# Kernel tuning notes

Hardware: AMD Instinct MI355X
Metric: run time of the kernel (lower is better)

## Reference

```python
import jax, jax.numpy as jnp
import numpy as np

B, S, D = 2, 2048, 1024
H, A = 16, 64  # num_heads, attention_dim


def setup_inputs() -> dict:
    key = jax.random.key(0)
    ks = jax.random.split(key, 9)
    sd = D ** -0.5
    so = (H * A) ** -0.5
    return {
        "x": jax.random.normal(ks[0], (B, S, D), dtype=jnp.float32),
        "Wq": jax.random.normal(ks[1], (D, H * A), dtype=jnp.float32) * sd,
        "bq": jnp.zeros((H * A,), dtype=jnp.float32),
        "Wk": jax.random.normal(ks[2], (D, H * A), dtype=jnp.float32) * sd,
        "bk": jnp.zeros((H * A,), dtype=jnp.float32),
        "Wv": jax.random.normal(ks[3], (D, H * A), dtype=jnp.float32) * sd,
        "bv": jnp.zeros((H * A,), dtype=jnp.float32),
        "Wo": jax.random.normal(ks[4], (H * A, D), dtype=jnp.float32) * so,
        "bo": jnp.zeros((D,), dtype=jnp.float32),
    }


def reference(x, Wq, bq, Wk, bk, Wv, bv, Wo, bo):
    b, s, _ = x.shape
    # project and split heads: [b, s, H, A]
    q = (x @ Wq + bq).reshape(b, s, H, A)
    k = (x @ Wk + bk).reshape(b, s, H, A)
    v = (x @ Wv + bv).reshape(b, s, H, A)
    # scores [b, H, s, s]
    scores = jnp.einsum("bqhd,bkhd->bhqk", q, k) / jnp.sqrt(jnp.float32(A))
    weights = jax.nn.softmax(scores, axis=-1)
    attended = jnp.einsum("bhqk,bkhd->bqhd", weights, v).reshape(b, s, H * A)
    return attended @ Wo + bo
```

## Files before the change

### kernel.cpp

```cpp
#include <hip/hip_runtime.h>
#include <hip/hip_bf16.h>

typedef __attribute__((ext_vector_type(8))) short bf16x8;
typedef __attribute__((ext_vector_type(4))) float f32x4;

#define LOG2E 1.44269504088896f

extern "C" __device__ float __ocml_native_exp2_f32(float);

__device__ __forceinline__ unsigned short f2bf(float f) {
    union { float f; unsigned int u; } v; v.f = f;
    unsigned int r = v.u + 0x7FFF + ((v.u >> 16) & 1);
    return (unsigned short)(r >> 16);
}

__device__ __forceinline__ unsigned int pk_bf16(float lo, float hi) {
    unsigned int r;
    asm("v_cvt_pk_bf16_f32 %0, %1, %2" : "=v"(r) : "v"(lo), "v"(hi));
    return r;
}

typedef __attribute__((address_space(3))) unsigned int lds_uint;
typedef __attribute__((address_space(1))) const unsigned int glob_uint;
__device__ __forceinline__ void gl2lds16(const void* g, void* l) {
    __builtin_amdgcn_global_load_lds((glob_uint*)g, (lds_uint*)l, 16, 0, 0);
}

__global__ __launch_bounds__(256) void cvt_bf16(const float* __restrict__ in,
                                                unsigned int* __restrict__ out, int n4) {
    int i = blockIdx.x * 256 + threadIdx.x;
    if (i >= n4) return;
    float4 v = ((const float4*)in)[i];
    uint2 o;
    o.x = pk_bf16(v.x, v.y);
    o.y = pk_bf16(v.z, v.w);
    ((uint2*)out)[i] = o;
}

__global__ __launch_bounds__(256) void transpose4_bf16(
    const float* __restrict__ w0, const float* __restrict__ w1,
    const float* __restrict__ w2, const float* __restrict__ w3,
    unsigned short* __restrict__ o0, unsigned short* __restrict__ o1,
    unsigned short* __restrict__ o2, unsigned short* __restrict__ o3) {
    const int z = blockIdx.z;
    const float* in = (z == 0) ? w0 : (z == 1) ? w1 : (z == 2) ? w2 : w3;
    unsigned short* out = (z == 0) ? o0 : (z == 1) ? o1 : (z == 2) ? o2 : o3;
    __shared__ float t[32][33];
    int tx = threadIdx.x & 31, ty = threadIdx.x >> 5;
    int r0 = blockIdx.y * 32, c0 = blockIdx.x * 32;
    for (int i = 0; i < 32; i += 8)
        t[ty + i][tx] = in[(size_t)(r0 + ty + i) * 1024 + c0 + tx];
    __syncthreads();
    for (int i = 0; i < 32; i += 8)
        out[(size_t)(c0 + ty + i) * 1024 + r0 + tx] = f2bf(t[tx][ty + i]);
}

__device__ __forceinline__ void gemm_core(const short* __restrict__ A,
                                          const short* __restrict__ BT,
                                          int K, int bm0, int bn0,
                                          short* As, short* Bs, f32x4 acc[4][4]) {
    const int tid = threadIdx.x;
    const int lane = tid & 63;
    const int w = tid >> 6;
    const int wr0 = (w >> 1) * 64;
    const int wc0 = (w & 1) * 64;
    const int l15 = lane & 15, quad = lane >> 4;
    const int sr = lane >> 2;
    const int slog = (lane & 3) ^ (sr & 3);

    for (int i = 0; i < 4; i++)
        for (int j = 0; j < 4; j++) acc[i][j] = (f32x4)0.f;

    for (int k0 = 0; k0 < K; k0 += 32) {
        for (int i = 0; i < 4; i++) {
            int c = w * 4 + i;
            if (c < 8)
                gl2lds16(A + (size_t)(bm0 + c * 16 + sr) * K + k0 + slog * 8,
                         As + c * 512);
            else
                gl2lds16(BT + (size_t)(bn0 + (c - 8) * 16 + sr) * K + k0 + slog * 8,
                         Bs + (c - 8) * 512);
        }
        __syncthreads();
        const int ph = (quad ^ (l15 & 3)) * 8;
        bf16x8 af[4], bfr[4];
        for (int im = 0; im < 4; im++)
            af[im] = *(const bf16x8*)&As[(wr0 + im * 16 + l15) * 32 + ph];
        for (int in = 0; in < 4; in++)
            bfr[in] = *(const bf16x8*)&Bs[(wc0 + in * 16 + l15) * 32 + ph];
        for (int im = 0; im < 4; im++)
            for (int in = 0; in < 4; in++)
                acc[im][in] = __builtin_amdgcn_mfma_f32_16x16x32_bf16(af[im], bfr[in], acc[im][in], 0, 0, 0);
        __syncthreads();
    }
}

__global__ __launch_bounds__(256) void gemm_qkv(
    const short* __restrict__ xb,
    const short* __restrict__ wqT, const short* __restrict__ wkT, const short* __restrict__ wvT,
    const float* __restrict__ bq, const float* __restrict__ bk, const float* __restrict__ bv,
    unsigned short* __restrict__ qb, unsigned short* __restrict__ kb, unsigned short* __restrict__ vTb) {
    __shared__ short As[4096], Bs[4096];
    const int z = blockIdx.z;
    const short* Amat = (z == 2) ? wvT : xb;
    const short* Bmat = (z == 0) ? wqT : (z == 1) ? wkT : xb;
    const float* bias = (z == 0) ? bq : (z == 1) ? bk : bv;
    const float scl = (z == 0) ? 0.125f * LOG2E : 1.f;
    const int bm0 = (z == 2) ? blockIdx.y * 128 : blockIdx.x * 128;
    const int bn0 = (z == 2) ? blockIdx.x * 128 : blockIdx.y * 128;
    f32x4 acc[4][4];
    gemm_core(Amat, Bmat, 1024, bm0, bn0, As, Bs, acc);
    const int lane = threadIdx.x & 63, w = threadIdx.x >> 6;
    const int wr0 = (w >> 1) * 64, wc0 = (w & 1) * 64, l15 = lane & 15, quad = lane >> 4;
    if (z == 2) {
        for (int im = 0; im < 4; im++)
            for (int in = 0; in < 4; in++)
                for (int r = 0; r < 4; r++) {
                    int rowa = bm0 + wr0 + im * 16 + quad * 4 + r;
                    int colg = bn0 + wc0 + in * 16 + l15;
                    unsigned short ov = f2bf(acc[im][in][r] + bias[rowa]);
                    int b = colg >> 11, s = colg & 2047;
                    vTb[(size_t)b * 2097152 + (size_t)rowa * 2048 + s] = ov;
                }
    } else {
        for (int im = 0; im < 4; im++)
            for (int in = 0; in < 4; in++)
                for (int r = 0; r < 4; r++) {
                    int rowg = bm0 + wr0 + im * 16 + quad * 4 + r;
                    int colg = bn0 + wc0 + in * 16 + l15;
                    unsigned short ov = f2bf((acc[im][in][r] + bias[colg]) * scl);
                    int b = rowg >> 11, s = rowg & 2047;
                    int h = colg >> 6, a = colg & 63;
                    int bh = b * 16 + h;
                    if (z == 0) qb[((size_t)bh * 2048 + s) * 64 + a] = ov;
                    else        kb[((size_t)bh * 2048 + s) * 64 + a] = ov;
                }
    }
}

__global__ __launch_bounds__(256) void gemm_out(
    const short* __restrict__ att, const short* __restrict__ woT,
    const float* __restrict__ bo, float* __restrict__ out) {
    __shared__ short As[4096], Bs[4096];
    const int bm0 = blockIdx.x * 128, bn0 = blockIdx.y * 128;
    f32x4 acc[4][4];
    gemm_core(att, woT, 1024, bm0, bn0, As, Bs, acc);
    const int lane = threadIdx.x & 63, w = threadIdx.x >> 6;
    const int wr0 = (w >> 1) * 64, wc0 = (w & 1) * 64, l15 = lane & 15, quad = lane >> 4;
    for (int im = 0; im < 4; im++)
        for (int in = 0; in < 4; in++)
            for (int r = 0; r < 4; r++) {
                int rowg = bm0 + wr0 + im * 16 + quad * 4 + r;
                int colg = bn0 + wc0 + in * 16 + l15;
                out[(size_t)rowg * 1024 + colg] = acc[im][in][r] + bo[colg];
            }
}

__global__ __launch_bounds__(512, 4) void flash_attn(
    const unsigned short* __restrict__ qb, const unsigned short* __restrict__ kb,
    const unsigned short* __restrict__ vTb, unsigned short* __restrict__ att) {
    __shared__ short Qs[8192];
    __shared__ short Ks[4][4096];
    __shared__ short Vs[4][4096];
    const int tid = threadIdx.x, lane = tid & 63, w = tid >> 6;
    const int l15 = lane & 15, quad = lane >> 4;
    const int q0 = blockIdx.x * 128;
    const int bh = blockIdx.y;
    const size_t qkbase = (size_t)bh * 2048 * 64;
    const size_t vbase = (size_t)bh * 64 * 2048;
    const int sr = lane >> 3;
    const int slog = (lane & 7) ^ sr;
    const int l7 = l15 & 7;

    const unsigned short* sgp;
    int sgstep, sg2;
    short* sgb;
    if (w < 4) {
        sgp = kb + qkbase + (size_t)(w * 16 + sr) * 64 + slog * 8;
        sgstep = 4096; sg2 = 512;
        sgb = &Ks[0][0] + w * 1024;
    } else {
        sgp = vTb + vbase + (size_t)((w - 4) * 16 + sr) * 2048 + slog * 8;
        sgstep = 64; sg2 = 16384;
        sgb = &Vs[0][0] + (w - 4) * 1024;
    }
    auto stage_tile = [&](int buf) {
        short* sd = sgb + buf * 4096;
        gl2lds16(sgp, sd);
        gl2lds16(sgp + sg2, sd + 512);
        sgp += sgstep;
    };

    for (int i = 0; i < 2; i++) {
        int c = w * 2 + i;
        gl2lds16(qb + qkbase + (size_t)(q0 + c * 8 + sr) * 64 + slog * 8, Qs + c * 512);
    }
    stage_tile(0); stage_tile(1); stage_tile(2);
    asm volatile("s_waitcnt vmcnt(4)" ::: "memory");
    __builtin_amdgcn_s_barrier();
    asm volatile("" ::: "memory");

    const int wq0 = w * 16;
    const int c0 = (quad ^ l7) * 8, c1 = c0 ^ 32;
    const int fb = l15 * 64;
    bf16x8 aq0 = *(const bf16x8*)&Qs[(wq0 + l15) * 64 + c0];
    bf16x8 aq1 = *(const bf16x8*)&Qs[(wq0 + l15) * 64 + c1];

    f32x4 o[4];
    for (int dt = 0; dt < 4; dt++) o[dt] = (f32x4)0.f;
    f32x4 ls = (f32x4)0.f;

    auto attn_step = [&](int buf) {
        const short* Kb = &Ks[0][0] + buf * 4096;
        const short* Vb = &Vs[0][0] + buf * 4096;
        f32x4 sc[4];
        __builtin_amdgcn_s_setprio(1);
#pragma unroll
        for (int t = 0; t < 4; t++) {
            bf16x8 ak = *(const bf16x8*)(Kb + fb + c0 + t * 1024);
            sc[t] = __builtin_amdgcn_mfma_f32_16x16x32_bf16(ak, aq0, (f32x4)0.f, 0, 0, 0);
        }
#pragma unroll
        for (int t = 0; t < 4; t++) {
            bf16x8 ak = *(const bf16x8*)(Kb + fb + c1 + t * 1024);
            sc[t] = __builtin_amdgcn_mfma_f32_16x16x32_bf16(ak, aq1, sc[t], 0, 0, 0);
        }
        __builtin_amdgcn_s_setprio(0);
#pragma unroll
        for (int t = 0; t < 4; t++) {
#pragma unroll
            for (int r = 0; r < 4; r++) sc[t][r] = __ocml_native_exp2_f32(sc[t][r]);
            ls += sc[t];
        }
        bf16x8 bp[2];
#pragma unroll
        for (int t2 = 0; t2 < 2; t2++) {
            unsigned pa = pk_bf16(sc[2 * t2][0], sc[2 * t2][1]);
            unsigned pb = pk_bf16(sc[2 * t2][2], sc[2 * t2][3]);
            unsigned pc = pk_bf16(sc[2 * t2 + 1][0], sc[2 * t2 + 1][1]);
            unsigned pd = pk_bf16(sc[2 * t2 + 1][2], sc[2 * t2 + 1][3]);
            asm("v_permlane32_swap_b32 %0, %1" : "+v"(pa), "+v"(pc));
            asm("v_permlane32_swap_b32 %0, %1" : "+v"(pb), "+v"(pd));
            asm("v_permlane16_swap_b32 %0, %1" : "+v"(pa), "+v"(pc));
            asm("v_permlane16_swap_b32 %0, %1" : "+v"(pb), "+v"(pd));
            union { unsigned u[4]; bf16x8 v; } cvt;
            cvt.u[0] = pa; cvt.u[1] = pb; cvt.u[2] = pc; cvt.u[3] = pd;
            bp[t2] = cvt.v;
        }
        __builtin_amdgcn_s_setprio(1);
#pragma unroll
        for (int t2 = 0; t2 < 2; t2++) {
            const int cc = t2 ? c1 : c0;
#pragma unroll
            for (int dt = 0; dt < 4; dt++) {
                bf16x8 av = *(const bf16x8*)(Vb + fb + cc + dt * 1024);
                o[dt] = __builtin_amdgcn_mfma_f32_16x16x32_bf16(av, bp[t2], o[dt], 0, 0, 0);
            }
        }
        __builtin_amdgcn_s_setprio(0);
    };

    for (int t = 0; t < 29; t++) {
        stage_tile((t + 3) & 3);
        attn_step(t & 3);
        asm volatile("s_waitcnt vmcnt(4)" ::: "memory");
        __builtin_amdgcn_s_barrier();
        asm volatile("" ::: "memory");
    }
    attn_step(1);
    asm volatile("s_waitcnt vmcnt(2)" ::: "memory");
    __builtin_amdgcn_s_barrier();
    asm volatile("" ::: "memory");
    attn_step(2);
    asm volatile("s_waitcnt vmcnt(0)" ::: "memory");
    __builtin_amdgcn_s_barrier();
    asm volatile("" ::: "memory");
    attn_step(3);

    const int b = bh >> 4, h = bh & 15;
    float l = (ls[0] + ls[1]) + (ls[2] + ls[3]);
    l += __shfl_xor(l, 16);
    l += __shfl_xor(l, 32);
    float inv = 1.f / l;
    int s = q0 + wq0 + l15;
    for (int dt = 0; dt < 4; dt++) {
        uint2 pk;
        pk.x = pk_bf16(o[dt][0] * inv, o[dt][1] * inv);
        pk.y = pk_bf16(o[dt][2] * inv, o[dt][3] * inv);
        int col = h * 64 + dt * 16 + quad * 4;
        *(uint2*)&att[((size_t)b * 2048 + s) * 1024 + col] = pk;
    }
}

extern "C" void kernel_launch(void* const* d_in, const int* in_sizes, int n_in,
                              void* d_out, int out_size, void* d_ws, size_t ws_size,
                              hipStream_t stream) {
    const float* x  = (const float*)d_in[0];
    const float* Wq = (const float*)d_in[1];
    const float* bq = (const float*)d_in[2];
    const float* Wk = (const float*)d_in[3];
    const float* bk = (const float*)d_in[4];
    const float* Wv = (const float*)d_in[5];
    const float* bv = (const float*)d_in[6];
    const float* Wo = (const float*)d_in[7];
    const float* bo = (const float*)d_in[8];
    float* out = (float*)d_out;

    short* ws  = (short*)d_ws;
    short* xb  = ws;
    short* wqT = ws + 4 * 1024 * 1024;
    short* wkT = wqT + 1024 * 1024;
    short* wvT = wkT + 1024 * 1024;
    short* woT = wvT + 1024 * 1024;
    short* qb  = woT + 1024 * 1024;
    short* kb  = qb + 4 * 1024 * 1024;
    short* vTb = kb + 4 * 1024 * 1024;
    short* att = vTb + 4 * 1024 * 1024;

    cvt_bf16<<<4096, 256, 0, stream>>>(x, (unsigned int*)xb, 1024 * 1024);
    transpose4_bf16<<<dim3(32, 32, 4), 256, 0, stream>>>(
        Wq, Wk, Wv, Wo,
        (unsigned short*)wqT, (unsigned short*)wkT,
        (unsigned short*)wvT, (unsigned short*)woT);
    gemm_qkv<<<dim3(32, 8, 3), 256, 0, stream>>>(xb, wqT, wkT, wvT, bq, bk, bv,
                                                 (unsigned short*)qb, (unsigned short*)kb,
                                                 (unsigned short*)vTb);
    flash_attn<<<dim3(16, 32), 512, 0, stream>>>((const unsigned short*)qb,
                                                 (const unsigned short*)kb,
                                                 (const unsigned short*)vTb,
                                                 (unsigned short*)att);
    gemm_out<<<dim3(32, 8), 256, 0, stream>>>(att, woT, bo, out);
}
```

Before: 200.3 us.

## Triple-buffer GEMM LDS tiles with async prefetch and extended swizzle

Rewrites the shared GEMM core used by the QKV and output projections so that global-to-LDS loads for later K tiles are issued while the current tile is computed. Three LDS buffers rotate, with vmcnt waits and one barrier per iteration replacing the two syncthreads per step. The LDS swizzle also folds in higher row bits to cut bank conflicts, and MFMA sections raise wave priority. The cost is triple the LDS per block, which may reduce occupancy, plus reliance on hand-placed waitcnt counts for correctness.

```diff
diff --git a/kernel.cpp b/kernel.cpp
--- a/kernel.cpp
+++ b/kernel.cpp
@@ -58,7 +58,7 @@
 __device__ __forceinline__ void gemm_core(const short* __restrict__ A,
                                           const short* __restrict__ BT,
                                           int K, int bm0, int bn0,
-                                          short* As, short* Bs, f32x4 acc[4][4]) {
+                                          short* sm, f32x4 acc[4][4]) {
     const int tid = threadIdx.x;
     const int lane = tid & 63;
     const int w = tid >> 6;
@@ -66,33 +66,69 @@
     const int wc0 = (w & 1) * 64;
     const int l15 = lane & 15, quad = lane >> 4;
     const int sr = lane >> 2;
-    const int slog = (lane & 3) ^ (sr & 3);
-
+    const int slog = (lane & 3) ^ (sr & 3) ^ (sr >> 2);
+
+#pragma unroll
     for (int i = 0; i < 4; i++)
+#pragma unroll
         for (int j = 0; j < 4; j++) acc[i][j] = (f32x4)0.f;
 
-    for (int k0 = 0; k0 < K; k0 += 32) {
+    const short* sp[4];
+    int sdo[4];
+#pragma unroll
+    for (int i = 0; i < 4; i++) {
+        int c = w * 4 + i;
+        sp[i] = (c < 8) ? A + (size_t)(bm0 + c * 16 + sr) * K + slog * 8
+                        : BT + (size_t)(bn0 + (c - 8) * 16 + sr) * K + slog * 8;
+        sdo[i] = c * 512;
+    }
+    auto stage = [&](int buf) {
+        short* bb = sm + buf * 8192;
+#pragma unroll
         for (int i = 0; i < 4; i++) {
-            int c = w * 4 + i;
-            if (c < 8)
-                gl2lds16(A + (size_t)(bm0 + c * 16 + sr) * K + k0 + slog * 8,
-                         As + c * 512);
-            else
-                gl2lds16(BT + (size_t)(bn0 + (c - 8) * 16 + sr) * K + k0 + slog * 8,
-                         Bs + (c - 8) * 512);
-        }
-        __syncthreads();
-        const int ph = (quad ^ (l15 & 3)) * 8;
+            gl2lds16(sp[i], bb + sdo[i]);
+            sp[i] += 32;
+        }
+    };
+    const int ph = (quad ^ (l15 & 3) ^ (l15 >> 2)) * 8;
+    auto compute = [&](int buf) {
+        const short* Ab = sm + buf * 8192;
+        const short* Bb = Ab + 4096;
         bf16x8 af[4], bfr[4];
+#pragma unroll
         for (int im = 0; im < 4; im++)
-            af[im] = *(const bf16x8*)&As[(wr0 + im * 16 + l15) * 32 + ph];
+            af[im] = *(const bf16x8*)&Ab[(wr0 + im * 16 + l15) * 32 + ph];
+#pragma unroll
         for (int in = 0; in < 4; in++)
-            bfr[in] = *(const bf16x8*)&Bs[(wc0 + in * 16 + l15) * 32 + ph];
+            bfr[in] = *(const bf16x8*)&Bb[(wc0 + in * 16 + l15) * 32 + ph];
+        __builtin_amdgcn_s_setprio(1);
+#pragma unroll
         for (int im = 0; im < 4; im++)
+#pragma unroll
             for (int in = 0; in < 4; in++)
                 acc[im][in] = __builtin_amdgcn_mfma_f32_16x16x32_bf16(af[im], bfr[in], acc[im][in], 0, 0, 0);
-        __syncthreads();
-    }
+        __builtin_amdgcn_s_setprio(0);
+    };
+
+    stage(0); stage(1);
+    asm volatile("s_waitcnt vmcnt(4)" ::: "memory");
+    __builtin_amdgcn_s_barrier();
+    asm volatile("" ::: "memory");
+
+    const int nt = K >> 5;
+    int bs = 2, bc = 0;
+    for (int t = 0; t < nt - 2; ++t) {
+        stage(bs); bs = (bs == 2) ? 0 : bs + 1;
+        compute(bc); bc = (bc == 2) ? 0 : bc + 1;
+        asm volatile("s_waitcnt vmcnt(4)" ::: "memory");
+        __builtin_amdgcn_s_barrier();
+        asm volatile("" ::: "memory");
+    }
+    compute(bc); bc = (bc == 2) ? 0 : bc + 1;
+    asm volatile("s_waitcnt vmcnt(0)" ::: "memory");
+    __builtin_amdgcn_s_barrier();
+    asm volatile("" ::: "memory");
+    compute(bc);
 }
 
 __global__ __launch_bounds__(256) void gemm_qkv(
@@ -100,7 +136,7 @@
     const short* __restrict__ wqT, const short* __restrict__ wkT, const short* __restrict__ wvT,
     const float* __restrict__ bq, const float* __restrict__ bk, const float* __restrict__ bv,
     unsigned short* __restrict__ qb, unsigned short* __restrict__ kb, unsigned short* __restrict__ vTb) {
-    __shared__ short As[4096], Bs[4096];
+    __shared__ short sm[24576];
     const int z = blockIdx.z;
     const short* Amat = (z == 2) ? wvT : xb;
     const short* Bmat = (z == 0) ? wqT : (z == 1) ? wkT : xb;
@@ -109,7 +145,7 @@
     const int bm0 = (z == 2) ? blockIdx.y * 128 : blockIdx.x * 128;
     const int bn0 = (z == 2) ? blockIdx.x * 128 : blockIdx.y * 128;
     f32x4 acc[4][4];
-    gemm_core(Amat, Bmat, 1024, bm0, bn0, As, Bs, acc);
+    gemm_core(Amat, Bmat, 1024, bm0, bn0, sm, acc);
     const int lane = threadIdx.x & 63, w = threadIdx.x >> 6;
     const int wr0 = (w >> 1) * 64, wc0 = (w & 1) * 64, l15 = lane & 15, quad = lane >> 4;
     if (z == 2) {
@@ -141,10 +177,10 @@
 __global__ __launch_bounds__(256) void gemm_out(
     const short* __restrict__ att, const short* __restrict__ woT,
     const float* __restrict__ bo, float* __restrict__ out) {
-    __shared__ short As[4096], Bs[4096];
+    __shared__ short sm[24576];
     const int bm0 = blockIdx.x * 128, bn0 = blockIdx.y * 128;
     f32x4 acc[4][4];
-    gemm_core(att, woT, 1024, bm0, bn0, As, Bs, acc);
+    gemm_core(att, woT, 1024, bm0, bn0, sm, acc);
     const int lane = threadIdx.x & 63, w = threadIdx.x >> 6;
     const int wr0 = (w >> 1) * 64, wc0 = (w & 1) * 64, l15 = lane & 15, quad = lane >> 4;
     for (int im = 0; im < 4; im++)
```

New measurement: 182.3 us. -9.0%, faster.
